# Performance work log

Hardware: AMD Instinct MI355X
Metric: run time of the kernel (lower is better)

Reference implementation:

```python
import jax, jax.numpy as jnp
import numpy as np

WS = 7    # window size
SS = 3    # shift size
NH = 6    # num heads
EPS = 1e-5


def _ln(x, g, b):
    m = jnp.mean(x, -1, keepdims=True)
    v = jnp.mean((x - m) ** 2, -1, keepdims=True)
    return (x - m) * jax.lax.rsqrt(v + EPS) * g + b


def _win_part(x, ws):
    # (B, H, W, C) -> (B*nW, ws*ws, C)
    B, H, W, C = x.shape
    x = x.reshape(B, H // ws, ws, W // ws, ws, C).transpose(0, 1, 3, 2, 4, 5)
    return x.reshape(-1, ws * ws, C)


def _win_rev(w, ws, B, H, W):
    # (B*nW, ws*ws, C) -> (B, H, W, C)
    C = w.shape[-1]
    x = w.reshape(B, H // ws, W // ws, ws, ws, C).transpose(0, 1, 3, 2, 4, 5)
    return x.reshape(B, H, W, C)


def _forward(x, norm1_g, norm1_b, qkv_w, qkv_b, proj_w, proj_b, norm2_g, norm2_b,
             fc1_w, fc1_b, fc2_w, fc2_b, rel_table, mask_matrix, H, W, rel_index):
    B, L, C = x.shape
    hd = C // NH
    shortcut = x
    h = _ln(x, norm1_g, norm1_b).reshape(B, H, W, C)
    pad_r = (WS - W % WS) % WS
    pad_b = (WS - H % WS) % WS
    h = jnp.pad(h, ((0, 0), (0, pad_b), (0, pad_r), (0, 0)))
    Hp, Wp = H + pad_b, W + pad_r
    # cyclic shift (shift_size > 0 path)
    h = jnp.roll(h, (-SS, -SS), axis=(1, 2))
    xw = _win_part(h, WS)                                   # [Bw, N, C]
    Bw, N, _ = xw.shape
    qkv = (xw @ qkv_w + qkv_b).reshape(Bw, N, 3, NH, hd)
    q = qkv[:, :, 0].transpose(0, 2, 1, 3) * (hd ** -0.5)   # [Bw, NH, N, hd]
    k = qkv[:, :, 1].transpose(0, 2, 1, 3)
    v = qkv[:, :, 2].transpose(0, 2, 1, 3)
    attn = q @ k.transpose(0, 1, 3, 2)                      # [Bw, NH, N, N]
    bias = rel_table[rel_index.reshape(-1)].reshape(N, N, NH).transpose(2, 0, 1)
    attn = attn + bias[None]
    nW = mask_matrix.shape[0]
    attn = attn.reshape(Bw // nW, nW, NH, N, N) + mask_matrix[None, :, None]
    attn = jax.nn.softmax(attn.reshape(Bw, NH, N, N), axis=-1)
    o = (attn @ v).transpose(0, 2, 1, 3).reshape(Bw, N, C)
    o = o @ proj_w + proj_b
    h = _win_rev(o, WS, B, Hp, Wp)
    h = jnp.roll(h, (SS, SS), axis=(1, 2))[:, :H, :W, :].reshape(B, L, C)
    x = shortcut + h
    y = _ln(x, norm2_g, norm2_b)
    y = jax.nn.gelu(y @ fc1_w + fc1_b, approximate=False) @ fc2_w + fc2_b  # torch GELU = exact erf
    return x + y


def setup_inputs() -> dict:
    B, H, W, C, HID = 32, 56, 56, 192, 768
    ws, ss = WS, SS
    ks = jax.random.split(jax.random.key(0), 8)
    rn = lambda i, shp, s: jax.random.normal(ks[i], shp, jnp.float32) * s
    inp = {
        'x': rn(0, (B, H * W, C), 1.0),
        'norm1_g': jnp.ones((C,), jnp.float32), 'norm1_b': jnp.zeros((C,), jnp.float32),
        'qkv_w': rn(1, (C, 3 * C), 0.02), 'qkv_b': jnp.zeros((3 * C,), jnp.float32),
        'proj_w': rn(2, (C, C), 0.02), 'proj_b': jnp.zeros((C,), jnp.float32),
        'norm2_g': jnp.ones((C,), jnp.float32), 'norm2_b': jnp.zeros((C,), jnp.float32),
        'fc1_w': rn(3, (C, HID), 0.02), 'fc1_b': jnp.zeros((HID,), jnp.float32),
        'fc2_w': rn(4, (HID, C), 0.02), 'fc2_b': jnp.zeros((C,), jnp.float32),
        'rel_table': rn(5, ((2 * ws - 1) ** 2, NH), 0.02),
    }
    # relative position index (same construction as torch buffer)
    coords = np.stack(np.meshgrid(np.arange(ws), np.arange(ws), indexing='ij')).reshape(2, -1)
    rel = (coords[:, :, None] - coords[:, None, :]).transpose(1, 2, 0)
    rel[..., 0] += ws - 1
    rel[..., 1] += ws - 1
    rel[..., 0] *= 2 * ws - 1
    inp['rel_index'] = jnp.asarray(rel.sum(-1), jnp.int32)  # [49, 49]
    # shifted-window attention mask (standard Swin construction)
    img = np.zeros((1, H, W, 1), np.float32)
    cnt = 0
    for hs in (slice(0, -ws), slice(-ws, -ss), slice(-ss, None)):
        for wsl in (slice(0, -ws), slice(-ws, -ss), slice(-ss, None)):
            img[:, hs, wsl, :] = cnt
            cnt += 1
    mw = img.reshape(1, H // ws, ws, W // ws, ws, 1).transpose(0, 1, 3, 2, 4, 5).reshape(-1, ws * ws)
    diff = mw[:, None, :] - mw[:, :, None]
    inp['mask_matrix'] = jnp.asarray(np.where(diff != 0, -100.0, 0.0), jnp.float32)  # [64, 49, 49]
    inp['H'] = H
    inp['W'] = W
    return inp


def reference(x, norm1_g, norm1_b, qkv_w, qkv_b, proj_w, proj_b, norm2_g, norm2_b,
              fc1_w, fc1_b, fc2_w, fc2_b, rel_table, rel_index, mask_matrix, H, W):
    return _forward(x, norm1_g, norm1_b, qkv_w, qkv_b, proj_w, proj_b, norm2_g, norm2_b,
                    fc1_w, fc1_b, fc2_w, fc2_b, rel_table, mask_matrix, H, W, rel_index)
```

## Files before the change

### kernel.cpp

```cpp
#include <hip/hip_runtime.h>

typedef __bf16 bf8 __attribute__((ext_vector_type(8)));
typedef float f4 __attribute__((ext_vector_type(4)));

__device__ __forceinline__ void stb(unsigned short* p, float v) { *(__bf16*)p = (__bf16)v; }

__device__ __forceinline__ void gl_lds16(const unsigned short* g, unsigned short* l) {
  __builtin_amdgcn_global_load_lds((const __attribute__((address_space(1))) unsigned int*)g,
                                   (__attribute__((address_space(3))) unsigned int*)l,
                                   16, 0, 0);
}

__device__ __forceinline__ float gelu_fast(float v) {
  float w = v * v;
  float u = v * (-1.59576912f - 0.07135481f * w);
  return v / (1.0f + __expf(u));
}

__global__ void transpose_kernel(const float* __restrict__ in,
                                 unsigned short* __restrict__ out, int K, int N) {
  int idx = blockIdx.x * 256 + threadIdx.x;
  if (idx < K * N) {
    int n = idx / K, k = idx - n * K;
    stb(&out[idx], in[k * N + n]);
  }
}

__global__ __launch_bounds__(256) void ln_kernel(const float* __restrict__ xin,
                                                 const float* __restrict__ g,
                                                 const float* __restrict__ bb,
                                                 unsigned short* __restrict__ out) {
  long token = (long)blockIdx.x * 4 + (threadIdx.x >> 6);
  int lane = threadIdx.x & 63;
  const float* row = xin + token * 192;
  float v[3] = {row[lane], row[lane + 64], row[lane + 128]};
  float s = v[0] + v[1] + v[2];
#pragma unroll
  for (int m = 1; m < 64; m <<= 1) s += __shfl_xor(s, m, 64);
  float mean = s * (1.0f / 192.0f);
  float d0 = v[0] - mean, d1 = v[1] - mean, d2 = v[2] - mean;
  float dd = d0 * d0 + d1 * d1 + d2 * d2;
#pragma unroll
  for (int m = 1; m < 64; m <<= 1) dd += __shfl_xor(dd, m, 64);
  float rstd = rsqrtf(dd * (1.0f / 192.0f) + 1e-5f);
  unsigned short* orow = out + token * 192;
#pragma unroll
  for (int i = 0; i < 3; i++) {
    int c = lane + i * 64;
    stb(&orow[c], (v[i] - mean) * rstd * g[c] + bb[c]);
  }
}

template <int EPI>
__global__ __launch_bounds__(256) void gemm_kernel(const unsigned short* __restrict__ A,
                                                   const unsigned short* __restrict__ Bt,
                                                   const float* __restrict__ bias,
                                                   const float* __restrict__ res,
                                                   void* __restrict__ out, int K, int N) {
  __shared__ __align__(16) unsigned short As[2][128 * 64];
  __shared__ __align__(16) unsigned short Bs[2][64 * 64];
  const int tid = threadIdx.x;
  const int wave = tid >> 6;
  const int lane = tid & 63;
  const int quad = lane >> 4;
  const int l16 = lane & 15;

  const int NX = gridDim.x;
  int lin = blockIdx.y * NX + blockIdx.x;
  const int T = NX * gridDim.y;
  if ((T & 7) == 0) {
    lin = (lin & 7) * (T >> 3) + (lin >> 3);
  }
  const int bx = lin % NX;
  const int by = lin / NX;
  const long m0 = (long)by * 128;
  const long n0 = (long)bx * 64;

  long a_src[4];
  int a_dstc[4];
#pragma unroll
  for (int j = 0; j < 4; ++j) {
    int L = (wave * 4 + j) * 64 + lane;
    int row = L >> 3, cs = L & 7;
    a_src[j] = (m0 + row) * (long)K + ((cs ^ (row & 7)) << 3);
    a_dstc[j] = (wave * 4 + j) * 512;
  }
  long b_src[2];
  int b_dstc[2];
#pragma unroll
  for (int j = 0; j < 2; ++j) {
    int L = (wave * 2 + j) * 64 + lane;
    int row = L >> 3, cs = L & 7;
    b_src[j] = (n0 + row) * (long)K + ((cs ^ (row & 7)) << 3);
    b_dstc[j] = (wave * 2 + j) * 512;
  }

  const int nT = K >> 6;
  f4 acc[2][4] = {};

#pragma unroll
  for (int j = 0; j < 4; ++j) gl_lds16(A + a_src[j], &As[0][a_dstc[j]]);
#pragma unroll
  for (int j = 0; j < 2; ++j) gl_lds16(Bt + b_src[j], &Bs[0][b_dstc[j]]);

  int cur = 0;
  for (int t = 0; t < nT; ++t) {
    if (t + 1 < nT) {
      const int k0 = (t + 1) << 6;
#pragma unroll
      for (int j = 0; j < 4; ++j) gl_lds16(A + a_src[j] + k0, &As[cur ^ 1][a_dstc[j]]);
#pragma unroll
      for (int j = 0; j < 2; ++j) gl_lds16(Bt + b_src[j] + k0, &Bs[cur ^ 1][b_dstc[j]]);
      asm volatile("s_waitcnt vmcnt(6)" ::: "memory");
    } else {
      asm volatile("s_waitcnt vmcnt(0)" ::: "memory");
    }
    __builtin_amdgcn_s_barrier();
    __builtin_amdgcn_sched_barrier(0);
#pragma unroll
    for (int kk = 0; kk < 2; ++kk) {
      bf8 a[2], b[4];
#pragma unroll
      for (int mt = 0; mt < 2; ++mt) {
        int r = wave * 32 + mt * 16 + l16;
        int c = kk * 4 + quad;
        a[mt] = *(const bf8*)&As[cur][r * 64 + ((c ^ (r & 7)) << 3)];
      }
#pragma unroll
      for (int nt = 0; nt < 4; ++nt) {
        int r = nt * 16 + l16;
        int c = kk * 4 + quad;
        b[nt] = *(const bf8*)&Bs[cur][r * 64 + ((c ^ (r & 7)) << 3)];
      }
#pragma unroll
      for (int mt = 0; mt < 2; ++mt)
#pragma unroll
        for (int nt = 0; nt < 4; ++nt)
          acc[mt][nt] = __builtin_amdgcn_mfma_f32_16x16x32_bf16(a[mt], b[nt], acc[mt][nt], 0, 0, 0);
    }
    __builtin_amdgcn_sched_barrier(0);
    __builtin_amdgcn_s_barrier();
    cur ^= 1;
  }

#pragma unroll
  for (int nt = 0; nt < 4; ++nt) {
    long n = n0 + nt * 16 + l16;
    float bv = bias[n];
#pragma unroll
    for (int mt = 0; mt < 2; ++mt) {
#pragma unroll
      for (int r = 0; r < 4; ++r) {
        long m = m0 + wave * 32 + mt * 16 + quad * 4 + r;
        float v = acc[mt][nt][r] + bv;
        long idx = m * N + n;
        if (EPI == 0) {
          stb(&((unsigned short*)out)[idx], v);
        } else if (EPI == 2) {
          stb(&((unsigned short*)out)[idx], gelu_fast(v));
        } else {
          ((float*)out)[idx] = v + res[idx];
        }
      }
    }
  }
}

__global__ __launch_bounds__(256) void proj_ln_kernel(const unsigned short* __restrict__ A,
                                                      const unsigned short* __restrict__ Bt,
                                                      const float* __restrict__ bias,
                                                      const float* __restrict__ res,
                                                      const float* __restrict__ g2,
                                                      const float* __restrict__ b2,
                                                      float* __restrict__ xres,
                                                      unsigned short* __restrict__ lnout) {
  __shared__ __align__(16) unsigned short As[2][128 * 64];
  __shared__ __align__(16) unsigned short Bs[2][192 * 64];
  const int tid = threadIdx.x;
  const int wave = tid >> 6;
  const int lane = tid & 63;
  const int quad = lane >> 4;
  const int l16 = lane & 15;

  int lin = blockIdx.y;
  const int T = gridDim.y;
  if ((T & 7) == 0) lin = (lin & 7) * (T >> 3) + (lin >> 3);
  const long m0 = (long)lin * 128;

  long a_src[4];
  int a_dstc[4];
#pragma unroll
  for (int j = 0; j < 4; ++j) {
    int L = (wave * 4 + j) * 64 + lane;
    int row = L >> 3, cs = L & 7;
    a_src[j] = (m0 + row) * 192L + ((cs ^ (row & 7)) << 3);
    a_dstc[j] = (wave * 4 + j) * 512;
  }
  long b_src[6];
  int b_dstc[6];
#pragma unroll
  for (int j = 0; j < 6; ++j) {
    int L = (wave * 6 + j) * 64 + lane;
    int row = L >> 3, cs = L & 7;
    b_src[j] = row * 192L + ((cs ^ (row & 7)) << 3);
    b_dstc[j] = (wave * 6 + j) * 512;
  }

  f4 acc[2][12] = {};

#pragma unroll
  for (int j = 0; j < 4; ++j) gl_lds16(A + a_src[j], &As[0][a_dstc[j]]);
#pragma unroll
  for (int j = 0; j < 6; ++j) gl_lds16(Bt + b_src[j], &Bs[0][b_dstc[j]]);

  int cur = 0;
  for (int t = 0; t < 3; ++t) {
    if (t + 1 < 3) {
      const int k0 = (t + 1) << 6;
#pragma unroll
      for (int j = 0; j < 4; ++j) gl_lds16(A + a_src[j] + k0, &As[cur ^ 1][a_dstc[j]]);
#pragma unroll
      for (int j = 0; j < 6; ++j) gl_lds16(Bt + b_src[j] + k0, &Bs[cur ^ 1][b_dstc[j]]);
      asm volatile("s_waitcnt vmcnt(10)" ::: "memory");
    } else {
      asm volatile("s_waitcnt vmcnt(0)" ::: "memory");
    }
    __builtin_amdgcn_s_barrier();
    __builtin_amdgcn_sched_barrier(0);
#pragma unroll
    for (int kk = 0; kk < 2; ++kk) {
      bf8 a[2];
#pragma unroll
      for (int mt = 0; mt < 2; ++mt) {
        int r = wave * 32 + mt * 16 + l16;
        int c = kk * 4 + quad;
        a[mt] = *(const bf8*)&As[cur][r * 64 + ((c ^ (r & 7)) << 3)];
      }
#pragma unroll
      for (int nt = 0; nt < 12; ++nt) {
        int r = nt * 16 + l16;
        int c = kk * 4 + quad;
        bf8 b = *(const bf8*)&Bs[cur][r * 64 + ((c ^ (r & 7)) << 3)];
#pragma unroll
        for (int mt = 0; mt < 2; ++mt)
          acc[mt][nt] = __builtin_amdgcn_mfma_f32_16x16x32_bf16(a[mt], b, acc[mt][nt], 0, 0, 0);
      }
    }
    __builtin_amdgcn_sched_barrier(0);
    __builtin_amdgcn_s_barrier();
    cur ^= 1;
  }

#pragma unroll
  for (int mt = 0; mt < 2; ++mt) {
#pragma unroll
    for (int r = 0; r < 4; ++r) {
      long mm = m0 + wave * 32 + mt * 16 + quad * 4 + r;
      const float* rrow = res + mm * 192;
      float v[12];
      float s = 0.0f;
#pragma unroll
      for (int nt = 0; nt < 12; ++nt) {
        int n = nt * 16 + l16;
        float t = acc[mt][nt][r] + bias[n] + rrow[n];
        v[nt] = t;
        s += t;
      }
#pragma unroll
      for (int m = 1; m < 16; m <<= 1) s += __shfl_xor(s, m, 64);
      float mean = s * (1.0f / 192.0f);
      float d = 0.0f;
#pragma unroll
      for (int nt = 0; nt < 12; ++nt) {
        float dd = v[nt] - mean;
        d += dd * dd;
      }
#pragma unroll
      for (int m = 1; m < 16; m <<= 1) d += __shfl_xor(d, m, 64);
      float rstd = rsqrtf(d * (1.0f / 192.0f) + 1e-5f);
      float* xrow = xres + mm * 192;
      unsigned short* lrow = lnout + mm * 192;
#pragma unroll
      for (int nt = 0; nt < 12; ++nt) {
        int n = nt * 16 + l16;
        xrow[n] = v[nt];
        stb(&lrow[n], (v[nt] - mean) * rstd * g2[n] + b2[n]);
      }
    }
  }
}

__global__ __launch_bounds__(128) void attn_kernel(const unsigned short* __restrict__ qkv,
                                                   const float* __restrict__ rel_t,
                                                   unsigned short* __restrict__ o) {
  __shared__ __align__(16) unsigned short sh[2 * 6912];
  __shared__ float relh[2][170];
  __shared__ int toksh[2][49];
  __shared__ int zsh[2][49];
  const int wave = threadIdx.x >> 6;
  const int lane = threadIdx.x & 63;
  const int quad = lane >> 4;
  const int l16 = lane & 15;
  const int p = blockIdx.x * 2 + wave;
  const int head = p % 6;
  const int wib = p / 6;
  const int wi = wib & 63;
  const int b = wib >> 6;
  unsigned short* Vts = sh + wave * 6912;
  unsigned short* Ps = Vts + 2304;

  if (lane < 49) {
    int r = lane / 7, c = lane - (lane / 7) * 7;
    int ph = (wi >> 3) * 7 + r, pw = (wi & 7) * 7 + c;
    int h = ph + 3; if (h >= 56) h -= 56;
    int w = pw + 3; if (w >= 56) w -= 56;
    toksh[wave][lane] = (b * 56 + h) * 56 + w;
    int zh = (ph < 49) ? 0 : (ph < 53 ? 1 : 2);
    int zw = (pw < 49) ? 0 : (pw < 53 ? 1 : 2);
    zsh[wave][lane] = zh * 3 + zw;
  }
  for (int i = lane; i < 169; i += 64) relh[wave][i] = rel_t[i * 6 + head];
  {
#pragma unroll
    for (int e = 0; e < 4; e++) {
      int ee = lane + e * 64;
      int d = ee >> 3, c8 = ee & 7;
      *(unsigned int*)&Vts[d * 72 + 48 + c8 * 2] = 0u;
    }
  }
  __syncthreads();

  for (int e = lane; e < 196; e += 64) {
    int n = e >> 2, c = e & 3;
    int t = toksh[wave][n];
    uint4 vc = *(const uint4*)(qkv + (long)t * 576 + head * 32 + 384 + c * 8);
    const unsigned short* vv = (const unsigned short*)&vc;
#pragma unroll
    for (int j = 0; j < 8; j++) Vts[(c * 8 + j) * 72 + n] = vv[j];
  }

  bf8 zv;
#pragma unroll
  for (int q8 = 0; q8 < 8; q8++) zv[q8] = (__bf16)0.0f;
  bf8 af[4], bf_[4];
#pragma unroll
  for (int i = 0; i < 4; i++) {
    int row = 16 * i + l16;
    int rv = row < 49 ? row : 48;
    long base = (long)toksh[wave][rv] * 576 + head * 32 + quad * 8;
    bf8 qf = *(const bf8*)(qkv + base);
    bf8 kf = *(const bf8*)(qkv + base + 192);
    if (row >= 49) { qf = zv; kf = zv; }
    af[i] = qf;
    bf_[i] = kf;
  }

  f4 S[4][4];
#pragma unroll
  for (int i = 0; i < 4; i++)
#pragma unroll
    for (int j = 0; j < 4; j++)
      S[i][j] = __builtin_amdgcn_mfma_f32_16x16x32_bf16(af[i], bf_[j], (f4){0.f, 0.f, 0.f, 0.f}, 0, 0, 0);

  int colv[4], colkey[4], zcol[4];
#pragma unroll
  for (int jt = 0; jt < 4; jt++) {
    int col = 16 * jt + l16;
    int cc = col < 49 ? col : 48;
    int rj = cc / 7, cj = cc - rj * 7;
    colkey[jt] = rj * 13 + cj;
    zcol[jt] = zsh[wave][cc];
    colv[jt] = (col < 49);
  }

  __syncthreads();

  const float sc = 0.17677669529663687f;
#pragma unroll
  for (int it = 0; it < 4; it++) {
#pragma unroll
    for (int r = 0; r < 4; r++) {
      int row = 16 * it + quad * 4 + r;
      int row2 = row < 49 ? row : 48;
      int ri = row2 / 7, ci = row2 - ri * 7;
      int rk = ri * 13 + ci + 84;
      int zr = zsh[wave][row2];
      float v[4];
#pragma unroll
      for (int jt = 0; jt < 4; jt++) {
        float bias = relh[wave][rk - colkey[jt]];
        float msk = (zr == zcol[jt]) ? 0.0f : -100.0f;
        float val = S[it][jt][r] * sc + bias + msk;
        v[jt] = colv[jt] ? val : -1e30f;
      }
      float mx = fmaxf(fmaxf(v[0], v[1]), fmaxf(v[2], v[3]));
#pragma unroll
      for (int m = 1; m < 16; m <<= 1) mx = fmaxf(mx, __shfl_xor(mx, m, 64));
      float e0 = __expf(v[0] - mx), e1 = __expf(v[1] - mx), e2 = __expf(v[2] - mx), e3 = __expf(v[3] - mx);
      float sum = e0 + e1 + e2 + e3;
#pragma unroll
      for (int m = 1; m < 16; m <<= 1) sum += __shfl_xor(sum, m, 64);
      float inv = 1.0f / sum;
      stb(&Ps[row * 72 + 0 + l16], e0 * inv);
      stb(&Ps[row * 72 + 16 + l16], e1 * inv);
      stb(&Ps[row * 72 + 32 + l16], e2 * inv);
      stb(&Ps[row * 72 + 48 + l16], e3 * inv);
    }
  }
  __syncthreads();

  f4 O[4][2] = {};
#pragma unroll
  for (int ks = 0; ks < 2; ks++) {
    bf8 pv[2];
#pragma unroll
    for (int nt = 0; nt < 2; nt++) pv[nt] = *(const bf8*)&Vts[(16 * nt + l16) * 72 + ks * 32 + quad * 8];
#pragma unroll
    for (int mt = 0; mt < 4; mt++) {
      bf8 pa = *(const bf8*)&Ps[(16 * mt + l16) * 72 + ks * 32 + quad * 8];
#pragma unroll
      for (int nt = 0; nt < 2; nt++)
        O[mt][nt] = __builtin_amdgcn_mfma_f32_16x16x32_bf16(pa, pv[nt], O[mt][nt], 0, 0, 0);
    }
  }
#pragma unroll
  for (int mt = 0; mt < 4; mt++) {
#pragma unroll
    for (int r = 0; r < 4; r++) {
      int row = 16 * mt + quad * 4 + r;
      if (row < 49) {
        long base = (long)toksh[wave][row] * 192 + head * 32 + l16;
        stb(&o[base], O[mt][0][r]);
        stb(&o[base + 16], O[mt][1][r]);
      }
    }
  }
}

extern "C" void kernel_launch(void* const* d_in, const int* in_sizes, int n_in,
                              void* d_out, int out_size, void* d_ws, size_t ws_size,
                              hipStream_t stream) {
  const float* x      = (const float*)d_in[0];
  const float* n1g    = (const float*)d_in[1];
  const float* n1b    = (const float*)d_in[2];
  const float* qkv_w  = (const float*)d_in[3];
  const float* qkv_b  = (const float*)d_in[4];
  const float* proj_w = (const float*)d_in[5];
  const float* proj_b = (const float*)d_in[6];
  const float* n2g    = (const float*)d_in[7];
  const float* n2b    = (const float*)d_in[8];
  const float* fc1_w  = (const float*)d_in[9];
  const float* fc1_b  = (const float*)d_in[10];
  const float* fc2_w  = (const float*)d_in[11];
  const float* fc2_b  = (const float*)d_in[12];
  const float* rel_t  = (const float*)d_in[13];
  const float* mask   = (const float*)d_in[15];
  (void)mask;

  char* ws = (char*)d_ws;
  unsigned short* qkv_wT  = (unsigned short*)(ws + 0);
  unsigned short* proj_wT = (unsigned short*)(ws + 221184);
  unsigned short* fc1_wT  = (unsigned short*)(ws + 294912);
  unsigned short* fc2_wT  = (unsigned short*)(ws + 589824);
  unsigned short* bufA    = (unsigned short*)(ws + 884736);
  unsigned short* bufB    = (unsigned short*)(ws + 39419904ULL);
  float*          xres    = (float*)(ws + 193560576ULL);

  const int M = 100352;

  transpose_kernel<<<(192 * 576 + 255) / 256, 256, 0, stream>>>(qkv_w, qkv_wT, 192, 576);
  transpose_kernel<<<(192 * 192 + 255) / 256, 256, 0, stream>>>(proj_w, proj_wT, 192, 192);
  transpose_kernel<<<(192 * 768 + 255) / 256, 256, 0, stream>>>(fc1_w, fc1_wT, 192, 768);
  transpose_kernel<<<(768 * 192 + 255) / 256, 256, 0, stream>>>(fc2_w, fc2_wT, 768, 192);

  ln_kernel<<<M / 4, 256, 0, stream>>>(x, n1g, n1b, bufA);
  gemm_kernel<0><<<dim3(576 / 64, M / 128), 256, 0, stream>>>(bufA, qkv_wT, qkv_b, nullptr, bufB, 192, 576);
  attn_kernel<<<12288 / 2, 128, 0, stream>>>(bufB, rel_t, bufA);
  proj_ln_kernel<<<dim3(1, M / 128), 256, 0, stream>>>(bufA, proj_wT, proj_b, x, n2g, n2b, xres, bufA);
  gemm_kernel<2><<<dim3(768 / 64, M / 128), 256, 0, stream>>>(bufA, fc1_wT, fc1_b, nullptr, bufB, 192, 768);
  gemm_kernel<3><<<dim3(192 / 64, M / 128), 256, 0, stream>>>(bufB, fc2_wT, fc2_b, xres, d_out, 768, 192);
}
```

Baseline: 504.6 us.

## Fuse fc1, GELU and fc2 into one MLP kernel keeping hidden activations on-chip

Replaces the separate fc1 and fc2 GEMM launches with one kernel. Each 128-row tile computes fc1 in 192-wide hidden chunks, applies GELU into LDS, and immediately accumulates fc2, so the 768-wide hidden tensor never goes to global memory. Weight tiles are double-buffered through LDS with direct global-to-LDS loads. The GELU approximation is rewritten with exp2 and a hardware reciprocal to use fewer instructions. The trade-off is large LDS use per block (about 144 KB), a 512-thread block, and only M/128 blocks, which may limit occupancy and parallelism.

```diff
diff --git a/kernel.cpp b/kernel.cpp
--- a/kernel.cpp
+++ b/kernel.cpp
@@ -13,8 +13,9 @@
 
 __device__ __forceinline__ float gelu_fast(float v) {
   float w = v * v;
-  float u = v * (-1.59576912f - 0.07135481f * w);
-  return v / (1.0f + __expf(u));
+  float u = v * (-2.30222655f - 0.10294296f * w);
+  float e = __builtin_amdgcn_exp2f(u);
+  return v * __builtin_amdgcn_rcpf(1.0f + e);
 }
 
 __global__ void transpose_kernel(const float* __restrict__ in,
@@ -286,6 +287,146 @@
         xrow[n] = v[nt];
         stb(&lrow[n], (v[nt] - mean) * rstd * g2[n] + b2[n]);
       }
+    }
+  }
+}
+
+__global__ __launch_bounds__(512) void mlp_kernel(const unsigned short* __restrict__ A,
+                                                  const unsigned short* __restrict__ W1t,
+                                                  const unsigned short* __restrict__ W2t,
+                                                  const float* __restrict__ b1,
+                                                  const float* __restrict__ b2,
+                                                  const float* __restrict__ res,
+                                                  float* __restrict__ out) {
+  __shared__ __align__(16) unsigned short As[128 * 192];
+  __shared__ __align__(16) unsigned short Bs[2][192 * 64];
+  __shared__ __align__(16) unsigned short Gs[8][16 * 200];
+  const int tid = threadIdx.x;
+  const int wave = tid >> 6;
+  const int lane = tid & 63;
+  const int quad = lane >> 4;
+  const int l16 = lane & 15;
+
+  int lin = blockIdx.x;
+  const int T = gridDim.x;
+  if ((T & 7) == 0) lin = (lin & 7) * (T >> 3) + (lin >> 3);
+  const long m0 = (long)lin * 128;
+
+#pragma unroll
+  for (int j = 0; j < 6; ++j) {
+    int L = (wave * 6 + j) * 64 + lane;
+    int row = L / 24;
+    int cs = L - row * 24;
+    long src = (m0 + row) * 192L + ((cs ^ (row & 7)) << 3);
+    gl_lds16(A + src, &As[(wave * 6 + j) * 512]);
+  }
+
+  int brow[3], bswz[3];
+#pragma unroll
+  for (int j = 0; j < 3; ++j) {
+    int L = (wave * 3 + j) * 64 + lane;
+    brow[j] = L >> 3;
+    int cs = L & 7;
+    bswz[j] = ((cs ^ (brow[j] & 7)) << 3);
+  }
+
+#define STAGE_B(c_, p_, kb_, buf_)                                            \
+  {                                                                           \
+    _Pragma("unroll") for (int j = 0; j < 3; ++j) {                           \
+      long src_;                                                              \
+      if (p_ == 0)                                                            \
+        src_ = (long)(c_) * 36864 + (long)brow[j] * 192 + (kb_) * 64 + bswz[j]; \
+      else                                                                    \
+        src_ = (long)brow[j] * 768 + (c_) * 192 + (kb_) * 64 + bswz[j];       \
+      gl_lds16(((p_) == 0 ? W1t : W2t) + src_, &Bs[buf_][(wave * 3 + j) * 512]); \
+    }                                                                         \
+  }
+
+  f4 oacc[12] = {};
+
+  STAGE_B(0, 0, 0, 0);
+
+  int cur = 0;
+  const int myrowA = (wave * 16 + l16) * 192;
+  const int swzl = l16 & 7;
+  unsigned short* Gmy = &Gs[wave][0];
+
+#pragma unroll 1
+  for (int c = 0; c < 4; ++c) {
+    f4 gacc[12] = {};
+#pragma unroll 1
+    for (int kb = 0; kb < 3; ++kb) {
+      if (kb < 2) {
+        STAGE_B(c, 0, kb + 1, cur ^ 1);
+      } else {
+        STAGE_B(c, 1, 0, cur ^ 1);
+      }
+      asm volatile("s_waitcnt vmcnt(3)" ::: "memory");
+      __builtin_amdgcn_s_barrier();
+      __builtin_amdgcn_sched_barrier(0);
+#pragma unroll
+      for (int kk = 0; kk < 2; ++kk) {
+        int csr = (kb * 2 + kk) * 4 + quad;
+        bf8 a = *(const bf8*)&As[myrowA + ((csr ^ swzl) << 3)];
+#pragma unroll
+        for (int nt = 0; nt < 12; ++nt) {
+          bf8 b = *(const bf8*)&Bs[cur][(nt * 16 + l16) * 64 + (((kk * 4 + quad) ^ swzl) << 3)];
+          gacc[nt] = __builtin_amdgcn_mfma_f32_16x16x32_bf16(a, b, gacc[nt], 0, 0, 0);
+        }
+      }
+      __builtin_amdgcn_sched_barrier(0);
+      __builtin_amdgcn_s_barrier();
+      cur ^= 1;
+    }
+#pragma unroll
+    for (int nt = 0; nt < 12; ++nt) {
+      float bv = b1[c * 192 + nt * 16 + l16];
+#pragma unroll
+      for (int r = 0; r < 4; ++r) {
+        float g = gelu_fast(gacc[nt][r] + bv);
+        stb(&Gmy[(quad * 4 + r) * 200 + nt * 16 + l16], g);
+      }
+    }
+    asm volatile("s_waitcnt lgkmcnt(0)" ::: "memory");
+    __builtin_amdgcn_sched_barrier(0);
+#pragma unroll 1
+    for (int kb = 0; kb < 3; ++kb) {
+      if (kb < 2) {
+        STAGE_B(c, 1, kb + 1, cur ^ 1);
+        asm volatile("s_waitcnt vmcnt(3)" ::: "memory");
+      } else if (c < 3) {
+        STAGE_B(c + 1, 0, 0, cur ^ 1);
+        asm volatile("s_waitcnt vmcnt(3)" ::: "memory");
+      } else {
+        asm volatile("s_waitcnt vmcnt(0)" ::: "memory");
+      }
+      __builtin_amdgcn_s_barrier();
+      __builtin_amdgcn_sched_barrier(0);
+#pragma unroll
+      for (int kk = 0; kk < 2; ++kk) {
+        bf8 a = *(const bf8*)&Gmy[l16 * 200 + (kb * 2 + kk) * 32 + quad * 8];
+#pragma unroll
+        for (int nt = 0; nt < 12; ++nt) {
+          bf8 b = *(const bf8*)&Bs[cur][(nt * 16 + l16) * 64 + (((kk * 4 + quad) ^ swzl) << 3)];
+          oacc[nt] = __builtin_amdgcn_mfma_f32_16x16x32_bf16(a, b, oacc[nt], 0, 0, 0);
+        }
+      }
+      __builtin_amdgcn_sched_barrier(0);
+      __builtin_amdgcn_s_barrier();
+      cur ^= 1;
+    }
+  }
+#undef STAGE_B
+
+#pragma unroll
+  for (int r = 0; r < 4; ++r) {
+    long mm = m0 + wave * 16 + quad * 4 + r;
+    const float* rrow = res + mm * 192;
+    float* orow = out + mm * 192;
+#pragma unroll
+    for (int nt = 0; nt < 12; ++nt) {
+      int n = nt * 16 + l16;
+      orow[n] = oacc[nt][r] + b2[n] + rrow[n];
     }
   }
 }
@@ -477,6 +618,5 @@
   gemm_kernel<0><<<dim3(576 / 64, M / 128), 256, 0, stream>>>(bufA, qkv_wT, qkv_b, nullptr, bufB, 192, 576);
   attn_kernel<<<12288 / 2, 128, 0, stream>>>(bufB, rel_t, bufA);
   proj_ln_kernel<<<dim3(1, M / 128), 256, 0, stream>>>(bufA, proj_wT, proj_b, x, n2g, n2b, xres, bufA);
-  gemm_kernel<2><<<dim3(768 / 64, M / 128), 256, 0, stream>>>(bufA, fc1_wT, fc1_b, nullptr, bufB, 192, 768);
-  gemm_kernel<3><<<dim3(192 / 64, M / 128), 256, 0, stream>>>(bufB, fc2_wT, fc2_b, xres, d_out, 768, 192);
-}
+  mlp_kernel<<<M / 128, 512, 0, stream>>>(bufA, fc1_wT, fc2_wT, fc1_b, fc2_b, xres, (float*)d_out);
+}
```

New measurement: 490.1 us. 2.9% less time.
